# Optimization experiments

Measured on AMD Instinct MI355X. Metric: run time of the kernel, lower is better.

Reference implementation:

```python
import jax, jax.numpy as jnp
import numpy as np

N = 8192      # total nodes
B = 8         # graphs in batch
L = 1024      # nodes per graph (max_len)
E = 262144    # edges (before self loops)
IN = 64       # in_channels
H = 8         # heads
C = 32        # hidden_channels (per-head out dim)
D = H * C     # 256, d_model
DFF = 2048    # transformer FFN dim (torch default)
NEG = -1e9


def setup_inputs() -> dict:
    key = jax.random.key(0)
    ks = jax.random.split(key, 24)
    def p(i, shape):
        return jax.random.normal(ks[i], shape, jnp.float32) * 0.02
    x = jax.random.normal(ks[0], (N, IN), jnp.float32)
    src = jax.random.randint(ks[1], (E,), 0, N)
    dst = (src // L) * L + jax.random.randint(ks[2], (E,), 0, L)  # keep edges within a graph
    edge_index = jnp.stack([src, dst]).astype(jnp.int32)
    batch = (jnp.arange(N) // L).astype(jnp.int32)
    return dict(
        x=x, edge_index=edge_index, batch=batch,
        gat_W0=p(3, (D, IN)), gat_W12=p(4, (2, D, D)),
        gat_att_src=p(5, (3, H, C)), gat_att_dst=p(6, (3, H, C)), gat_bias=p(7, (3, D)),
        tf_qkv_w=p(8, (2, 3 * D, D)), tf_qkv_b=p(9, (2, 3 * D)),
        tf_out_w=p(10, (2, D, D)), tf_out_b=p(11, (2, D)),
        tf_ln1_w=jnp.ones((2, D)), tf_ln1_b=jnp.zeros((2, D)),
        tf_ln2_w=jnp.ones((2, D)), tf_ln2_b=jnp.zeros((2, D)),
        tf_ff1_w=p(12, (2, DFF, D)), tf_ff1_b=p(13, (2, DFF)),
        tf_ff2_w=p(14, (2, D, DFF)), tf_ff2_b=p(15, (2, D)),
        pred_w=p(16, (3, D)), pred_b=p(17, (3,)),
    )


def _gat(x, src, dst, W, att_s, att_d, bias):
    # PyG GATConv, concat=True, add_self_loops (appended in caller), eval (no dropout)
    h = (x @ W.T).reshape(-1, H, C)                       # [N,H,C]
    a_s = (h * att_s).sum(-1)                             # [N,H]
    a_d = (h * att_d).sum(-1)
    e = jax.nn.leaky_relu(a_s[src] + a_d[dst], 0.2)       # [E+N,H]
    m = jax.ops.segment_max(e, dst, num_segments=N)       # per-dst softmax
    e = jnp.exp(e - m[dst])
    s = jax.ops.segment_sum(e, dst, num_segments=N)
    alpha = e / s[dst]
    out = jax.ops.segment_sum(h[src] * alpha[..., None], dst, num_segments=N)
    return out.reshape(-1, D) + bias


def _ln(x, w, b):
    mu = x.mean(-1, keepdims=True)
    v = ((x - mu) ** 2).mean(-1, keepdims=True)
    return (x - mu) / jnp.sqrt(v + 1e-5) * w + b


def _tf_layer(x, mask, qkv_w, qkv_b, out_w, out_b, ln1w, ln1b, ln2w, ln2b, f1w, f1b, f2w, f2b):
    # torch TransformerEncoderLayer (post-LN, relu), key padding mask, eval mode
    qkv = x @ qkv_w.T + qkv_b                              # [B,L,3D]
    q, k, v = jnp.split(qkv, 3, -1)
    sh = lambda t: t.reshape(B, L, H, D // H)
    q, k, v = sh(q), sh(k), sh(v)
    sc = jnp.einsum('bqhd,bkhd->bhqk', q, k) * (1.0 / float(np.sqrt(D // H)))
    sc = jnp.where(mask[:, None, None, :], NEG, sc)
    a = jax.nn.softmax(sc, -1)
    o = jnp.einsum('bhqk,bkhd->bqhd', a, v).reshape(B, L, D)
    x = _ln(x + o @ out_w.T + out_b, ln1w, ln1b)
    f = jax.nn.relu(x @ f1w.T + f1b) @ f2w.T + f2b
    return _ln(x + f, ln2w, ln2b)


def reference(x, edge_index, batch, gat_W0, gat_W12, gat_att_src, gat_att_dst, gat_bias,
              tf_qkv_w, tf_qkv_b, tf_out_w, tf_out_b, tf_ln1_w, tf_ln1_b, tf_ln2_w, tf_ln2_b,
              tf_ff1_w, tf_ff1_b, tf_ff2_w, tf_ff2_b, pred_w, pred_b):
    loops = jnp.arange(N, dtype=edge_index.dtype)
    src = jnp.concatenate([edge_index[0], loops])
    dst = jnp.concatenate([edge_index[1], loops])
    h = jax.nn.relu(_gat(x, src, dst, gat_W0, gat_att_src[0], gat_att_dst[0], gat_bias[0]))
    for i in range(2):
        h = jax.nn.relu(_gat(h, src, dst, gat_W12[i], gat_att_src[i + 1], gat_att_dst[i + 1], gat_bias[i + 1]))
    # ragged -> padded [B, L, D] (vectorized scatter instead of python loop)
    seq_lens = jax.ops.segment_sum(jnp.ones(N, jnp.int32), batch, num_segments=B)
    starts = jnp.cumsum(seq_lens) - seq_lens
    pos = jnp.arange(N) - starts[batch]
    xp = jnp.zeros((B, L, D), h.dtype).at[batch, pos].set(h)
    mask = jnp.arange(L)[None, :] >= seq_lens[:, None]     # True = padded key
    for i in range(2):
        xp = _tf_layer(xp, mask, tf_qkv_w[i], tf_qkv_b[i], tf_out_w[i], tf_out_b[i],
                       tf_ln1_w[i], tf_ln1_b[i], tf_ln2_w[i], tf_ln2_b[i],
                       tf_ff1_w[i], tf_ff1_b[i], tf_ff2_w[i], tf_ff2_b[i])
    return xp @ pred_w.T + pred_b                          # [B,L,3]
```

## Files before the change

kernel.cpp:

```cpp
#include <hip/hip_runtime.h>
#include <hip/hip_bf16.h>

#define NN 8192
#define EE 262144
#define BB 8
#define LL 1024
#define HH 8
#define DD 256
#define DFFN 2048

typedef short s8v __attribute__((ext_vector_type(8)));
typedef float f32x4 __attribute__((ext_vector_type(4)));
typedef unsigned short ushort;

__device__ inline ushort f2bf(float f) {
    unsigned u = __float_as_uint(f);
    u = (u + 0x7fffu + ((u >> 16) & 1u)) >> 16;
    return (ushort)u;
}
__device__ inline float bf2f(ushort u) {
    return __uint_as_float(((unsigned)u) << 16);
}

template<bool BIAS, bool RELU, bool RES, bool WF, bool WB>
__global__ __launch_bounds__(256) void mgemm_kernel(
    const ushort* __restrict__ A, const ushort* __restrict__ W,
    const float* __restrict__ bias, const float* __restrict__ res,
    float* __restrict__ Cf, ushort* __restrict__ Cb, int M, int N, int K)
{
    __shared__ ushort As[128 * 32];
    __shared__ ushort Bs[128 * 32];
    int t = threadIdx.x;
    int l = t & 63;
    int quad = l >> 4, l15 = l & 15;
    int swz = (l15 >> 1) & 3;
    int rq = (quad ^ swz) * 8;
    int w = t >> 6;
    int wm = (w >> 1) * 64, wn = (w & 1) * 64;
    int m0 = blockIdx.x * 128, n0 = blockIdx.y * 128;

    f32x4 z = {0.f, 0.f, 0.f, 0.f};
    f32x4 acc[4][4];
#pragma unroll
    for (int i = 0; i < 4; ++i)
#pragma unroll
        for (int j = 0; j < 4; ++j) acc[i][j] = z;

    for (int k0 = 0; k0 < K; k0 += 32) {
#pragma unroll
        for (int i = 0; i < 2; ++i) {
            int chunk = i * 256 + t;
            int r = chunk >> 2, q = chunk & 3;
            int qs = (q ^ ((r >> 1) & 3)) * 8;
            __builtin_amdgcn_global_load_lds(
                (const __attribute__((address_space(1))) unsigned int*)
                    (A + (size_t)(m0 + r) * K + k0 + qs),
                (__attribute__((address_space(3))) unsigned int*)(As + chunk * 8), 16, 0, 0);
            __builtin_amdgcn_global_load_lds(
                (const __attribute__((address_space(1))) unsigned int*)
                    (W + (size_t)(n0 + r) * K + k0 + qs),
                (__attribute__((address_space(3))) unsigned int*)(Bs + chunk * 8), 16, 0, 0);
        }
        __syncthreads();
        s8v af[4], bfv[4];
#pragma unroll
        for (int i = 0; i < 4; ++i) {
            af[i]  = *(const s8v*)(As + (wm + i * 16 + l15) * 32 + rq);
            bfv[i] = *(const s8v*)(Bs + (wn + i * 16 + l15) * 32 + rq);
        }
#pragma unroll
        for (int mi = 0; mi < 4; ++mi)
#pragma unroll
            for (int ni = 0; ni < 4; ++ni)
                acc[mi][ni] = __builtin_amdgcn_mfma_f32_16x16x32_bf16(
                    af[mi], bfv[ni], acc[mi][ni], 0, 0, 0);
        __syncthreads();
    }

#pragma unroll
    for (int mi = 0; mi < 4; ++mi) {
#pragma unroll
        for (int ni = 0; ni < 4; ++ni) {
            int n = n0 + wn + ni * 16 + l15;
#pragma unroll
            for (int r = 0; r < 4; ++r) {
                int m = m0 + wm + mi * 16 + quad * 4 + r;
                float v = acc[mi][ni][r];
                if (BIAS) v += bias[n];
                if (RES)  v += res[(size_t)m * N + n];
                if (RELU) v = fmaxf(v, 0.f);
                if (WF) Cf[(size_t)m * N + n] = v;
                if (WB) Cb[(size_t)m * N + n] = f2bf(v);
            }
        }
    }
}

template<bool BIAS, bool RELU, bool RES, bool WF, bool WB, bool ASD>
__global__ __launch_bounds__(256) void mgemm64_kernel(
    const ushort* __restrict__ A, const ushort* __restrict__ W,
    const float* __restrict__ bias, const float* __restrict__ res,
    float* __restrict__ Cf, ushort* __restrict__ Cb,
    const float* __restrict__ atts, const float* __restrict__ attd,
    float* __restrict__ a_s, float* __restrict__ a_d, int M, int N, int K)
{
    __shared__ ushort As[64 * 32];
    __shared__ ushort Bs[64 * 32];
    int t = threadIdx.x;
    int l = t & 63;
    int quad = l >> 4, l15 = l & 15;
    int rq = (quad ^ ((l15 >> 1) & 3)) * 8;
    int w = t >> 6;
    int wm = (w >> 1) * 32, wn = (w & 1) * 32;
    int m0 = blockIdx.x * 64, n0 = blockIdx.y * 64;

    f32x4 z = {0.f, 0.f, 0.f, 0.f};
    f32x4 acc[2][2];
#pragma unroll
    for (int i = 0; i < 2; ++i)
#pragma unroll
        for (int j = 0; j < 2; ++j) acc[i][j] = z;

    for (int k0 = 0; k0 < K; k0 += 32) {
        {
            int r = t >> 2, q = t & 3;
            int qs = (q ^ ((r >> 1) & 3)) * 8;
            __builtin_amdgcn_global_load_lds(
                (const __attribute__((address_space(1))) unsigned int*)
                    (A + (size_t)(m0 + r) * K + k0 + qs),
                (__attribute__((address_space(3))) unsigned int*)(As + t * 8), 16, 0, 0);
            __builtin_amdgcn_global_load_lds(
                (const __attribute__((address_space(1))) unsigned int*)
                    (W + (size_t)(n0 + r) * K + k0 + qs),
                (__attribute__((address_space(3))) unsigned int*)(Bs + t * 8), 16, 0, 0);
        }
        __syncthreads();
        s8v af[2], bfv[2];
#pragma unroll
        for (int i = 0; i < 2; ++i) {
            af[i]  = *(const s8v*)(As + (wm + i * 16 + l15) * 32 + rq);
            bfv[i] = *(const s8v*)(Bs + (wn + i * 16 + l15) * 32 + rq);
        }
#pragma unroll
        for (int mi = 0; mi < 2; ++mi)
#pragma unroll
            for (int ni = 0; ni < 2; ++ni)
                acc[mi][ni] = __builtin_amdgcn_mfma_f32_16x16x32_bf16(
                    af[mi], bfv[ni], acc[mi][ni], 0, 0, 0);
        __syncthreads();
    }

#pragma unroll
    for (int mi = 0; mi < 2; ++mi) {
#pragma unroll
        for (int ni = 0; ni < 2; ++ni) {
            int n = n0 + wn + ni * 16 + l15;
#pragma unroll
            for (int r = 0; r < 4; ++r) {
                int m = m0 + wm + mi * 16 + quad * 4 + r;
                float v = acc[mi][ni][r];
                if (BIAS) v += bias[n];
                if (RES)  v += res[(size_t)m * N + n];
                if (RELU) v = fmaxf(v, 0.f);
                if (WF) Cf[(size_t)m * N + n] = v;
                if (WB) Cb[(size_t)m * N + n] = f2bf(v);
            }
        }
    }

    if (ASD) {
        int head = ((n0 + wn) >> 5) & 7;
        float as0 = atts[head * 32 + l15];
        float as1 = atts[head * 32 + 16 + l15];
        float ad0 = attd[head * 32 + l15];
        float ad1 = attd[head * 32 + 16 + l15];
#pragma unroll
        for (int mi = 0; mi < 2; ++mi)
#pragma unroll
            for (int r = 0; r < 4; ++r) {
                float sp = acc[mi][0][r] * as0 + acc[mi][1][r] * as1;
                float dp = acc[mi][0][r] * ad0 + acc[mi][1][r] * ad1;
#pragma unroll
                for (int off = 1; off < 16; off <<= 1) {
                    sp += __shfl_xor(sp, off);
                    dp += __shfl_xor(dp, off);
                }
                if (l15 == 0) {
                    int m = m0 + wm + mi * 16 + quad * 4 + r;
                    a_s[m * 8 + head] = sp;
                    a_d[m * 8 + head] = dp;
                }
            }
    }
}

__global__ __launch_bounds__(256) void mgemm_qkv_kernel(
    const ushort* __restrict__ A, const ushort* __restrict__ W,
    const float* __restrict__ bias,
    ushort* __restrict__ Qb, ushort* __restrict__ Kb, ushort* __restrict__ Vt,
    int M, int K)
{
    __shared__ ushort As[128 * 32];
    __shared__ ushort Bs[128 * 32];
    int t = threadIdx.x;
    int l = t & 63;
    int quad = l >> 4, l15 = l & 15;
    int swz = (l15 >> 1) & 3;
    int rq = (quad ^ swz) * 8;
    int w = t >> 6;
    int wm = (w >> 1) * 64, wn = (w & 1) * 64;
    int m0 = blockIdx.x * 128, n0 = blockIdx.y * 128;

    f32x4 z = {0.f, 0.f, 0.f, 0.f};
    f32x4 acc[4][4];
#pragma unroll
    for (int i = 0; i < 4; ++i)
#pragma unroll
        for (int j = 0; j < 4; ++j) acc[i][j] = z;

    for (int k0 = 0; k0 < K; k0 += 32) {
#pragma unroll
        for (int i = 0; i < 2; ++i) {
            int chunk = i * 256 + t;
            int r = chunk >> 2, q = chunk & 3;
            int qs = (q ^ ((r >> 1) & 3)) * 8;
            __builtin_amdgcn_global_load_lds(
                (const __attribute__((address_space(1))) unsigned int*)
                    (A + (size_t)(m0 + r) * K + k0 + qs),
                (__attribute__((address_space(3))) unsigned int*)(As + chunk * 8), 16, 0, 0);
            __builtin_amdgcn_global_load_lds(
                (const __attribute__((address_space(1))) unsigned int*)
                    (W + (size_t)(n0 + r) * K + k0 + qs),
                (__attribute__((address_space(3))) unsigned int*)(Bs + chunk * 8), 16, 0, 0);
        }
        __syncthreads();
        s8v af[4], bfv[4];
#pragma unroll
        for (int i = 0; i < 4; ++i) {
            af[i]  = *(const s8v*)(As + (wm + i * 16 + l15) * 32 + rq);
            bfv[i] = *(const s8v*)(Bs + (wn + i * 16 + l15) * 32 + rq);
        }
#pragma unroll
        for (int mi = 0; mi < 4; ++mi)
#pragma unroll
            for (int ni = 0; ni < 4; ++ni)
                acc[mi][ni] = __builtin_amdgcn_mfma_f32_16x16x32_bf16(
                    af[mi], bfv[ni], acc[mi][ni], 0, 0, 0);
        __syncthreads();
    }

#pragma unroll
    for (int mi = 0; mi < 4; ++mi) {
#pragma unroll
        for (int ni = 0; ni < 4; ++ni) {
            int n = n0 + wn + ni * 16 + l15;
            int sec = n >> 8, hc = n & 255;
            int hh = hc >> 5, c = hc & 31;
            float bv = bias[n];
#pragma unroll
            for (int r = 0; r < 4; ++r) {
                int m = m0 + wm + mi * 16 + quad * 4 + r;
                float v = acc[mi][ni][r] + bv;
                int b = m >> 10, ll2 = m & 1023;
                int bh = b * 8 + hh;
                if (sec == 0)
                    Qb[(size_t)bh * 32768 + ll2 * 32 + c] = f2bf(v * 0.17677669529663687f);
                else if (sec == 1)
                    Kb[(size_t)bh * 32768 + ll2 * 32 + c] = f2bf(v);
                else
                    Vt[(size_t)bh * 32768 + c * 1024 + ll2] = f2bf(v);
            }
        }
    }
}

__global__ __launch_bounds__(256) void castall_kernel(
    const float* __restrict__ W0, const float* __restrict__ W12,
    const float* __restrict__ qkvw, const float* __restrict__ outw,
    const float* __restrict__ f1w, const float* __restrict__ f2w,
    const float* __restrict__ x,
    ushort* __restrict__ W0b, ushort* __restrict__ W12b,
    ushort* __restrict__ qkvb, ushort* __restrict__ outb,
    ushort* __restrict__ f1b, ushort* __restrict__ f2b,
    ushort* __restrict__ xb, int* __restrict__ deg)
{
    int tid = blockIdx.x * 256 + threadIdx.x;
    if (tid < 2048) *(int4*)(deg + tid * 4) = make_int4(0, 0, 0, 0);
    int e = tid * 4;
    if (e >= 3293184) return;
    const float* s; ushort* d; int off;
    if (e < 16384)        { s = W0;   d = W0b;  off = e; }
    else if (e < 147456)  { s = W12;  d = W12b; off = e - 16384; }
    else if (e < 540672)  { s = qkvw; d = qkvb; off = e - 147456; }
    else if (e < 671744)  { s = outw; d = outb; off = e - 540672; }
    else if (e < 1720320) { s = f1w;  d = f1b;  off = e - 671744; }
    else if (e < 2768896) { s = f2w;  d = f2b;  off = e - 1720320; }
    else                  { s = x;    d = xb;   off = e - 2768896; }
    float4 v = *(const float4*)(s + off);
    d[off + 0] = f2bf(v.x); d[off + 1] = f2bf(v.y);
    d[off + 2] = f2bf(v.z); d[off + 3] = f2bf(v.w);
}

__global__ void count_kernel(const int* __restrict__ ei, int* __restrict__ deg)
{
    int e = blockIdx.x * 256 + threadIdx.x;
    if (e >= EE + NN) return;
    int d = (e < EE) ? ei[EE + e] : (e - EE);
    atomicAdd(&deg[d], 1);
}

__global__ __launch_bounds__(1024) void scan_kernel(
    const int* __restrict__ deg, int* __restrict__ rowptr, int* __restrict__ cursor)
{
    __shared__ int part[1024];
    int t = threadIdx.x;
    int base = t * 8;
    int loc[8]; int s = 0;
#pragma unroll
    for (int i = 0; i < 8; ++i) { loc[i] = deg[base + i]; s += loc[i]; }
    part[t] = s;
    __syncthreads();
    for (int off = 1; off < 1024; off <<= 1) {
        int v = (t >= off) ? part[t - off] : 0;
        __syncthreads();
        part[t] += v;
        __syncthreads();
    }
    int run = (t == 0) ? 0 : part[t - 1];
#pragma unroll
    for (int i = 0; i < 8; ++i) { rowptr[base + i] = run; cursor[base + i] = run; run += loc[i]; }
    if (t == 1023) rowptr[NN] = run;
}

__global__ void scatter_kernel(const int* __restrict__ ei, int* __restrict__ cursor,
                               int* __restrict__ col)
{
    int e = blockIdx.x * 256 + threadIdx.x;
    if (e >= EE + NN) return;
    int s, d;
    if (e < EE) { s = ei[e]; d = ei[EE + e]; } else { s = e - EE; d = s; }
    int slot = atomicAdd(&cursor[d], 1);
    col[slot] = s;
}

__global__ __launch_bounds__(256) void gat_agg_kernel(
    const ushort* __restrict__ hlinb, const float* __restrict__ a_s,
    const float* __restrict__ a_d, const int* __restrict__ rowptr,
    const int* __restrict__ col, const float* __restrict__ bias,
    float* __restrict__ alpha_e,
    float* __restrict__ out, ushort* __restrict__ outb)
{
    int wid = threadIdx.x >> 6, lane = threadIdx.x & 63;
    int dst = blockIdx.x * 4 + wid;
    int start = rowptr[dst], end = rowptr[dst + 1];
    float ad[HH];
#pragma unroll
    for (int h = 0; h < HH; ++h) ad[h] = a_d[(size_t)dst * HH + h];

    float sm[HH];
#pragma unroll
    for (int h = 0; h < HH; ++h) sm[h] = 0.f;
    for (int e = start + lane; e < end; e += 64) {
        int s = col[e];
        float* al = alpha_e + (size_t)e * HH;
#pragma unroll
        for (int h = 0; h < HH; ++h) {
            float v = a_s[(size_t)s * HH + h] + ad[h];
            v = v > 0.f ? v : 0.2f * v;
            float p = __expf(v);
            sm[h] += p;
            al[h] = p;
        }
    }
#pragma unroll
    for (int h = 0; h < HH; ++h)
#pragma unroll
        for (int off = 32; off; off >>= 1) sm[h] += __shfl_xor(sm[h], off);

    int myh = lane >> 3;
    float invs = 1.f / sm[myh];
    float a0 = 0.f, a1 = 0.f, a2 = 0.f, a3 = 0.f;
    for (int e = start; e < end; ++e) {
        int s = col[e];
        float alpha = alpha_e[(size_t)e * HH + myh] * invs;
        uint2 hv = *(const uint2*)(hlinb + (size_t)s * DD + lane * 4);
        a0 += alpha * bf2f((ushort)(hv.x & 0xffff));
        a1 += alpha * bf2f((ushort)(hv.x >> 16));
        a2 += alpha * bf2f((ushort)(hv.y & 0xffff));
        a3 += alpha * bf2f((ushort)(hv.y >> 16));
    }
    float4 bv = *(const float4*)(bias + lane * 4);
    float r0 = fmaxf(a0 + bv.x, 0.f);
    float r1 = fmaxf(a1 + bv.y, 0.f);
    float r2 = fmaxf(a2 + bv.z, 0.f);
    float r3 = fmaxf(a3 + bv.w, 0.f);
    float* op = out + (size_t)dst * DD + lane * 4;
    op[0] = r0; op[1] = r1; op[2] = r2; op[3] = r3;
    ushort* ob = outb + (size_t)dst * DD + lane * 4;
    ob[0] = f2bf(r0); ob[1] = f2bf(r1); ob[2] = f2bf(r2); ob[3] = f2bf(r3);
}

__global__ __launch_bounds__(256, 4) void attn_flash_kernel(
    const ushort* __restrict__ Qb, const ushort* __restrict__ Kb,
    const ushort* __restrict__ Vt, ushort* __restrict__ outb)
{
    __shared__ ushort Ks[128 * 32];
    __shared__ ushort Vs[32 * 128];
    __shared__ ushort pw[4][16][132];

    int t = threadIdx.x;
    int w = t >> 6, lane = t & 63;
    int quad = lane >> 4, l15 = lane & 15;
    int kq = (quad ^ ((l15 >> 1) & 3)) * 8;
    int bh = blockIdx.y;
    int q0 = blockIdx.x * 64 + w * 16;
    int b = bh >> 3, h = bh & 7;

    const ushort* qbase = Qb + (size_t)bh * 32768;
    const ushort* kbase = Kb + (size_t)bh * 32768;
    const ushort* vbase = Vt + (size_t)bh * 32768;

    s8v aq = *(const s8v*)(qbase + (q0 + l15) * 32 + quad * 8);

    f32x4 z = {0.f, 0.f, 0.f, 0.f};
    f32x4 o0 = z, o1 = z;
    float lden[4] = {0.f, 0.f, 0.f, 0.f};

    for (int ch = 0; ch < 8; ++ch) {
        int j0 = ch * 128;
#pragma unroll
        for (int i = 0; i < 2; ++i) {
            int idx = i * 256 + t;
            int kr = idx >> 2, kc = idx & 3;
            int kcs = (kc ^ ((kr >> 1) & 3)) * 8;
            __builtin_amdgcn_global_load_lds(
                (const __attribute__((address_space(1))) unsigned int*)
                    (kbase + (size_t)(j0 + kr) * 32 + kcs),
                (__attribute__((address_space(3))) unsigned int*)(Ks + idx * 8), 16, 0, 0);
            int vr = idx >> 4, vc = idx & 15;
            int vcs = (vc ^ (vr & 15)) * 8;
            __builtin_amdgcn_global_load_lds(
                (const __attribute__((address_space(1))) unsigned int*)
                    (vbase + (size_t)vr * 1024 + j0 + vcs),
                (__attribute__((address_space(3))) unsigned int*)(Vs + idx * 8), 16, 0, 0);
        }
        __syncthreads();

        f32x4 s[8];
#pragma unroll
        for (int kk = 0; kk < 8; ++kk) {
            s8v bk = *(const s8v*)(Ks + (kk * 16 + l15) * 32 + kq);
            s[kk] = __builtin_amdgcn_mfma_f32_16x16x32_bf16(aq, bk, z, 0, 0, 0);
        }

        float cs[4] = {0.f, 0.f, 0.f, 0.f};
#pragma unroll
        for (int kk = 0; kk < 8; ++kk) {
#pragma unroll
            for (int r = 0; r < 4; ++r) {
                float p = __expf(s[kk][r]);
                cs[r] += p;
                pw[w][quad * 4 + r][kk * 16 + l15] = f2bf(p);
            }
        }
#pragma unroll
        for (int r = 0; r < 4; ++r) {
#pragma unroll
            for (int off = 1; off < 16; off <<= 1) cs[r] += __shfl_xor(cs[r], off);
            lden[r] += cs[r];
        }

#pragma unroll
        for (int kk = 0; kk < 4; ++kk) {
            s8v ap = *(const s8v*)(&pw[w][l15][kk * 32 + quad * 8]);
            int c0 = ((kk * 4 + quad) ^ l15) * 8;
            s8v b0 = *(const s8v*)(Vs + (size_t)l15 * 128 + c0);
            s8v b1 = *(const s8v*)(Vs + (size_t)(16 + l15) * 128 + c0);
            o0 = __builtin_amdgcn_mfma_f32_16x16x32_bf16(ap, b0, o0, 0, 0, 0);
            o1 = __builtin_amdgcn_mfma_f32_16x16x32_bf16(ap, b1, o1, 0, 0, 0);
        }
        __syncthreads();
    }

#pragma unroll
    for (int r = 0; r < 4; ++r) {
        int row = q0 + quad * 4 + r;
        float inv = 1.f / lden[r];
        outb[(size_t)(b * 1024 + row) * 256 + h * 32 + l15]      = f2bf(o0[r] * inv);
        outb[(size_t)(b * 1024 + row) * 256 + h * 32 + 16 + l15] = f2bf(o1[r] * inv);
    }
}

__global__ __launch_bounds__(256) void ln_kernel(
    float* __restrict__ x, const float* __restrict__ w, const float* __restrict__ b,
    ushort* __restrict__ xb)
{
    int wid = threadIdx.x >> 6, lane = threadIdx.x & 63;
    size_t row = blockIdx.x * 4 + wid;
    float4 v = *(float4*)(x + row * DD + lane * 4);
    float s = v.x + v.y + v.z + v.w;
#pragma unroll
    for (int off = 32; off; off >>= 1) s += __shfl_xor(s, off);
    float mu = s * (1.f / 256.f);
    float dx = v.x - mu, dy = v.y - mu, dz = v.z - mu, dw = v.w - mu;
    float q = dx * dx + dy * dy + dz * dz + dw * dw;
#pragma unroll
    for (int off = 32; off; off >>= 1) q += __shfl_xor(q, off);
    float rstd = rsqrtf(q * (1.f / 256.f) + 1e-5f);
    int c = lane * 4;
    float4 wv = *(const float4*)(w + c);
    float4 bv = *(const float4*)(b + c);
    float4 o;
    o.x = dx * rstd * wv.x + bv.x;
    o.y = dy * rstd * wv.y + bv.y;
    o.z = dz * rstd * wv.z + bv.z;
    o.w = dw * rstd * wv.w + bv.w;
    *(float4*)(x + row * DD + c) = o;
    ushort* ob = xb + row * DD + c;
    ob[0] = f2bf(o.x); ob[1] = f2bf(o.y); ob[2] = f2bf(o.z); ob[3] = f2bf(o.w);
}

__global__ __launch_bounds__(256) void ln_pred_kernel(
    const float* __restrict__ x, const float* __restrict__ w, const float* __restrict__ b,
    const float* __restrict__ pw, const float* __restrict__ pb,
    float* __restrict__ out)
{
    int wid = threadIdx.x >> 6, lane = threadIdx.x & 63;
    size_t row = blockIdx.x * 4 + wid;
    float4 v = *(const float4*)(x + row * DD + lane * 4);
    float s = v.x + v.y + v.z + v.w;
#pragma unroll
    for (int off = 32; off; off >>= 1) s += __shfl_xor(s, off);
    float mu = s * (1.f / 256.f);
    float dx = v.x - mu, dy = v.y - mu, dz = v.z - mu, dw = v.w - mu;
    float q = dx * dx + dy * dy + dz * dz + dw * dw;
#pragma unroll
    for (int off = 32; off; off >>= 1) q += __shfl_xor(q, off);
    float rstd = rsqrtf(q * (1.f / 256.f) + 1e-5f);
    int c = lane * 4;
    float4 wv = *(const float4*)(w + c);
    float4 bv = *(const float4*)(b + c);
    float4 o;
    o.x = dx * rstd * wv.x + bv.x;
    o.y = dy * rstd * wv.y + bv.y;
    o.z = dz * rstd * wv.z + bv.z;
    o.w = dw * rstd * wv.w + bv.w;
    float4 w0 = *(const float4*)(pw + c);
    float4 w1 = *(const float4*)(pw + DD + c);
    float4 w2 = *(const float4*)(pw + 2 * DD + c);
    float s0 = o.x * w0.x + o.y * w0.y + o.z * w0.z + o.w * w0.w;
    float s1 = o.x * w1.x + o.y * w1.y + o.z * w1.z + o.w * w1.w;
    float s2 = o.x * w2.x + o.y * w2.y + o.z * w2.z + o.w * w2.w;
#pragma unroll
    for (int off = 32; off; off >>= 1) {
        s0 += __shfl_xor(s0, off);
        s1 += __shfl_xor(s1, off);
        s2 += __shfl_xor(s2, off);
    }
    if (lane == 0) {
        out[row * 3 + 0] = s0 + pb[0];
        out[row * 3 + 1] = s1 + pb[1];
        out[row * 3 + 2] = s2 + pb[2];
    }
}

extern "C" void kernel_launch(void* const* d_in, const int* in_sizes, int n_in,
                              void* d_out, int out_size, void* d_ws, size_t ws_size,
                              hipStream_t stream)
{
    const float* x        = (const float*)d_in[0];
    const int*   ei       = (const int*)d_in[1];
    const float* gat_W0   = (const float*)d_in[3];
    const float* gat_W12  = (const float*)d_in[4];
    const float* att_src  = (const float*)d_in[5];
    const float* att_dst  = (const float*)d_in[6];
    const float* gat_bias = (const float*)d_in[7];
    const float* qkv_w    = (const float*)d_in[8];
    const float* qkv_b    = (const float*)d_in[9];
    const float* out_w    = (const float*)d_in[10];
    const float* out_b    = (const float*)d_in[11];
    const float* ln1_w    = (const float*)d_in[12];
    const float* ln1_b    = (const float*)d_in[13];
    const float* ln2_w    = (const float*)d_in[14];
    const float* ln2_b    = (const float*)d_in[15];
    const float* ff1_w    = (const float*)d_in[16];
    const float* ff1_b    = (const float*)d_in[17];
    const float* ff2_w    = (const float*)d_in[18];
    const float* ff2_b    = (const float*)d_in[19];
    const float* pred_w   = (const float*)d_in[20];
    const float* pred_b   = (const float*)d_in[21];
    float* outp = (float*)d_out;

    float* ws   = (float*)d_ws;
    float* hA   = ws;
    float* hB   = ws + 2097152;
    ushort* ffb  = (ushort*)(ws + 4194304);
    ushort* Qb   = (ushort*)(ws + 12582912);
    ushort* Kb   = (ushort*)(ws + 13631488);
    ushort* Vt   = (ushort*)(ws + 14680064);
    ushort* attnb= (ushort*)(ws + 15728640);
    ushort* lnb  = (ushort*)(ws + 16777216);
    ushort* hBb  = (ushort*)(ws + 17825792);
    ushort* xb   = (ushort*)(ws + 18874368);
    ushort* wbase= (ushort*)(ws + 19136512);
    ushort* W0b    = wbase;
    ushort* W12b   = wbase + 16384;
    ushort* qkv_wb = wbase + 147456;
    ushort* out_wb = wbase + 540672;
    ushort* ff1_wb = wbase + 671744;
    ushort* ff2_wb = wbase + 1720320;
    float* a_s  = ws + 20520960;
    float* a_d  = ws + 20586496;
    int*   iw   = (int*)(ws + 20652032);
    int*   deg    = iw;
    int*   rowptr = iw + 8192;
    int*   cursor = iw + 16392;
    int*   col    = iw + 24592;
    ushort* hAb    = (ushort*)(ws + 21000192);
    float*  alpha_e = ws + 22048768;

    castall_kernel<<<3216, 256, 0, stream>>>(
        gat_W0, gat_W12, qkv_w, out_w, ff1_w, ff2_w, x,
        W0b, W12b, qkv_wb, out_wb, ff1_wb, ff2_wb, xb, deg);

    int etot = EE + NN;
    count_kernel<<<(etot + 255) / 256, 256, 0, stream>>>(ei, deg);
    scan_kernel<<<1, 1024, 0, stream>>>(deg, rowptr, cursor);
    scatter_kernel<<<(etot + 255) / 256, 256, 0, stream>>>(ei, cursor, col);

    mgemm64_kernel<false, false, false, false, true, true><<<dim3(128, 4), 256, 0, stream>>>(
        xb, W0b, nullptr, nullptr, nullptr, hAb, att_src, att_dst, a_s, a_d, NN, DD, 64);
    gat_agg_kernel<<<2048, 256, 0, stream>>>(hAb, a_s, a_d, rowptr, col, gat_bias,
                                             alpha_e, hB, hBb);

    for (int l = 0; l < 2; ++l) {
        mgemm64_kernel<false, false, false, false, true, true><<<dim3(128, 4), 256, 0, stream>>>(
            hBb, W12b + (size_t)l * DD * DD, nullptr, nullptr, nullptr, hAb,
            att_src + (l + 1) * 256, att_dst + (l + 1) * 256, a_s, a_d, NN, DD, DD);
        gat_agg_kernel<<<2048, 256, 0, stream>>>(
            hAb, a_s, a_d, rowptr, col, gat_bias + (l + 1) * 256, alpha_e, hB, hBb);
    }

    for (int l = 0; l < 2; ++l) {
        mgemm_qkv_kernel<<<dim3(64, 6), 256, 0, stream>>>(
            hBb, qkv_wb + (size_t)l * 768 * DD, qkv_b + l * 768, Qb, Kb, Vt, NN, DD);
        attn_flash_kernel<<<dim3(16, 64), 256, 0, stream>>>(Qb, Kb, Vt, attnb);
        mgemm64_kernel<true, false, true, true, false, false><<<dim3(128, 4), 256, 0, stream>>>(
            attnb, out_wb + (size_t)l * DD * DD, out_b + l * DD, hB,
            hA, nullptr, nullptr, nullptr, nullptr, nullptr, NN, DD, DD);
        ln_kernel<<<2048, 256, 0, stream>>>(hA, ln1_w + l * DD, ln1_b + l * DD, lnb);
        mgemm_kernel<true, true, false, false, true><<<dim3(64, 16), 256, 0, stream>>>(
            lnb, ff1_wb + (size_t)l * DFFN * DD, ff1_b + l * DFFN, nullptr,
            nullptr, ffb, NN, DFFN, DD);
        mgemm64_kernel<true, false, true, true, false, false><<<dim3(128, 4), 256, 0, stream>>>(
            ffb, ff2_wb + (size_t)l * DD * DFFN, ff2_b + l * DD, hA,
            hB, nullptr, nullptr, nullptr, nullptr, nullptr, NN, DD, DFFN);
        if (l == 0) {
            ln_kernel<<<2048, 256, 0, stream>>>(hB, ln2_w + l * DD, ln2_b + l * DD, hBb);
        } else {
            ln_pred_kernel<<<2048, 256, 0, stream>>>(
                hB, ln2_w + l * DD, ln2_b + l * DD, pred_w, pred_b, outp);
        }
    }
}
```

Measured before the change: 471.6 us.

## Retile GEMMs to K=64 steps and process 32 query rows per attention wave

Result: faster. 451.7 us (-4.2%).

```diff
diff --git a/kernel.cpp b/kernel.cpp
--- a/kernel.cpp
+++ b/kernel.cpp
@@ -104,12 +104,12 @@
     const float* __restrict__ atts, const float* __restrict__ attd,
     float* __restrict__ a_s, float* __restrict__ a_d, int M, int N, int K)
 {
-    __shared__ ushort As[64 * 32];
-    __shared__ ushort Bs[64 * 32];
+    __shared__ ushort As[64 * 64];
+    __shared__ ushort Bs[64 * 64];
     int t = threadIdx.x;
     int l = t & 63;
     int quad = l >> 4, l15 = l & 15;
-    int rq = (quad ^ ((l15 >> 1) & 3)) * 8;
+    int r7 = l15 & 7;
     int w = t >> 6;
     int wm = (w >> 1) * 32, wn = (w & 1) * 32;
     int m0 = blockIdx.x * 64, n0 = blockIdx.y * 64;
@@ -121,32 +121,39 @@
 #pragma unroll
         for (int j = 0; j < 2; ++j) acc[i][j] = z;
 
-    for (int k0 = 0; k0 < K; k0 += 32) {
-        {
-            int r = t >> 2, q = t & 3;
-            int qs = (q ^ ((r >> 1) & 3)) * 8;
+    for (int k0 = 0; k0 < K; k0 += 64) {
+#pragma unroll
+        for (int i = 0; i < 2; ++i) {
+            int chunk = i * 256 + t;
+            int r = chunk >> 3, p = chunk & 7;
+            int qs = (p ^ (r & 7)) * 8;
             __builtin_amdgcn_global_load_lds(
                 (const __attribute__((address_space(1))) unsigned int*)
                     (A + (size_t)(m0 + r) * K + k0 + qs),
-                (__attribute__((address_space(3))) unsigned int*)(As + t * 8), 16, 0, 0);
+                (__attribute__((address_space(3))) unsigned int*)(As + chunk * 8), 16, 0, 0);
             __builtin_amdgcn_global_load_lds(
                 (const __attribute__((address_space(1))) unsigned int*)
                     (W + (size_t)(n0 + r) * K + k0 + qs),
-                (__attribute__((address_space(3))) unsigned int*)(Bs + t * 8), 16, 0, 0);
-        }
-        __syncthreads();
-        s8v af[2], bfv[2];
-#pragma unroll
-        for (int i = 0; i < 2; ++i) {
-            af[i]  = *(const s8v*)(As + (wm + i * 16 + l15) * 32 + rq);
-            bfv[i] = *(const s8v*)(Bs + (wn + i * 16 + l15) * 32 + rq);
-        }
-#pragma unroll
-        for (int mi = 0; mi < 2; ++mi)
-#pragma unroll
-            for (int ni = 0; ni < 2; ++ni)
-                acc[mi][ni] = __builtin_amdgcn_mfma_f32_16x16x32_bf16(
-                    af[mi], bfv[ni], acc[mi][ni], 0, 0, 0);
+                (__attribute__((address_space(3))) unsigned int*)(Bs + chunk * 8), 16, 0, 0);
+        }
+        __syncthreads();
+#pragma unroll
+        for (int kk = 0; kk < 2; ++kk) {
+            s8v af[2], bfv[2];
+            int c = kk * 4 + quad;
+            int off = (c ^ r7) * 8;
+#pragma unroll
+            for (int i = 0; i < 2; ++i) {
+                af[i]  = *(const s8v*)(As + (wm + i * 16 + l15) * 64 + off);
+                bfv[i] = *(const s8v*)(Bs + (wn + i * 16 + l15) * 64 + off);
+            }
+#pragma unroll
+            for (int mi = 0; mi < 2; ++mi)
+#pragma unroll
+                for (int ni = 0; ni < 2; ++ni)
+                    acc[mi][ni] = __builtin_amdgcn_mfma_f32_16x16x32_bf16(
+                        af[mi], bfv[ni], acc[mi][ni], 0, 0, 0);
+        }
         __syncthreads();
     }
 
@@ -200,30 +207,29 @@
     ushort* __restrict__ Qb, ushort* __restrict__ Kb, ushort* __restrict__ Vt,
     int M, int K)
 {
-    __shared__ ushort As[128 * 32];
-    __shared__ ushort Bs[128 * 32];
+    __shared__ ushort As[64 * 64];
+    __shared__ ushort Bs[64 * 64];
     int t = threadIdx.x;
     int l = t & 63;
     int quad = l >> 4, l15 = l & 15;
-    int swz = (l15 >> 1) & 3;
-    int rq = (quad ^ swz) * 8;
+    int r7 = l15 & 7;
     int w = t >> 6;
-    int wm = (w >> 1) * 64, wn = (w & 1) * 64;
-    int m0 = blockIdx.x * 128, n0 = blockIdx.y * 128;
+    int wm = (w >> 1) * 32, wn = (w & 1) * 32;
+    int m0 = blockIdx.x * 64, n0 = blockIdx.y * 64;
 
     f32x4 z = {0.f, 0.f, 0.f, 0.f};
-    f32x4 acc[4][4];
-#pragma unroll
-    for (int i = 0; i < 4; ++i)
-#pragma unroll
-        for (int j = 0; j < 4; ++j) acc[i][j] = z;
-
-    for (int k0 = 0; k0 < K; k0 += 32) {
+    f32x4 acc[2][2];
+#pragma unroll
+    for (int i = 0; i < 2; ++i)
+#pragma unroll
+        for (int j = 0; j < 2; ++j) acc[i][j] = z;
+
+    for (int k0 = 0; k0 < K; k0 += 64) {
 #pragma unroll
         for (int i = 0; i < 2; ++i) {
             int chunk = i * 256 + t;
-            int r = chunk >> 2, q = chunk & 3;
-            int qs = (q ^ ((r >> 1) & 3)) * 8;
+            int r = chunk >> 3, p = chunk & 7;
+            int qs = (p ^ (r & 7)) * 8;
             __builtin_amdgcn_global_load_lds(
                 (const __attribute__((address_space(1))) unsigned int*)
                     (A + (size_t)(m0 + r) * K + k0 + qs),
@@ -234,25 +240,30 @@
                 (__attribute__((address_space(3))) unsigned int*)(Bs + chunk * 8), 16, 0, 0);
         }
         __syncthreads();
-        s8v af[4], bfv[4];
-#pragma unroll
-        for (int i = 0; i < 4; ++i) {
-            af[i]  = *(const s8v*)(As + (wm + i * 16 + l15) * 32 + rq);
-            bfv[i] = *(const s8v*)(Bs + (wn + i * 16 + l15) * 32 + rq);
-        }
-#pragma unroll
-        for (int mi = 0; mi < 4; ++mi)
-#pragma unroll
-            for (int ni = 0; ni < 4; ++ni)
-                acc[mi][ni] = __builtin_amdgcn_mfma_f32_16x16x32_bf16(
-                    af[mi], bfv[ni], acc[mi][ni], 0, 0, 0);
-        __syncthreads();
-    }
-
-#pragma unroll
-    for (int mi = 0; mi < 4; ++mi) {
-#pragma unroll
-        for (int ni = 0; ni < 4; ++ni) {
+#pragma unroll
+        for (int kk = 0; kk < 2; ++kk) {
+            s8v af[2], bfv[2];
+            int c = kk * 4 + quad;
+            int off = (c ^ r7) * 8;
+#pragma unroll
+            for (int i = 0; i < 2; ++i) {
+                af[i]  = *(const s8v*)(As + (wm + i * 16 + l15) * 64 + off);
+                bfv[i] = *(const s8v*)(Bs + (wn + i * 16 + l15) * 64 + off);
+            }
+#pragma unroll
+            for (int mi = 0; mi < 2; ++mi)
+#pragma unroll
+                for (int ni = 0; ni < 2; ++ni)
+                    acc[mi][ni] = __builtin_amdgcn_mfma_f32_16x16x32_bf16(
+                        af[mi], bfv[ni], acc[mi][ni], 0, 0, 0);
+        }
+        __syncthreads();
+    }
+
+#pragma unroll
+    for (int mi = 0; mi < 2; ++mi) {
+#pragma unroll
+        for (int ni = 0; ni < 2; ++ni) {
             int n = n0 + wn + ni * 16 + l15;
             int sec = n >> 8, hc = n & 255;
             int hh = hc >> 5, c = hc & 31;
@@ -400,31 +411,33 @@
     ob[0] = f2bf(r0); ob[1] = f2bf(r1); ob[2] = f2bf(r2); ob[3] = f2bf(r3);
 }
 
-__global__ __launch_bounds__(256, 4) void attn_flash_kernel(
+__global__ __launch_bounds__(256, 2) void attn_flash_kernel(
     const ushort* __restrict__ Qb, const ushort* __restrict__ Kb,
     const ushort* __restrict__ Vt, ushort* __restrict__ outb)
 {
     __shared__ ushort Ks[128 * 32];
     __shared__ ushort Vs[32 * 128];
-    __shared__ ushort pw[4][16][132];
+    __shared__ ushort pw[4][32][132];
 
     int t = threadIdx.x;
     int w = t >> 6, lane = t & 63;
     int quad = lane >> 4, l15 = lane & 15;
     int kq = (quad ^ ((l15 >> 1) & 3)) * 8;
     int bh = blockIdx.y;
-    int q0 = blockIdx.x * 64 + w * 16;
+    int q0 = blockIdx.x * 128 + w * 32;
     int b = bh >> 3, h = bh & 7;
 
     const ushort* qbase = Qb + (size_t)bh * 32768;
     const ushort* kbase = Kb + (size_t)bh * 32768;
     const ushort* vbase = Vt + (size_t)bh * 32768;
 
-    s8v aq = *(const s8v*)(qbase + (q0 + l15) * 32 + quad * 8);
+    s8v aq0 = *(const s8v*)(qbase + (q0 + l15) * 32 + quad * 8);
+    s8v aq1 = *(const s8v*)(qbase + (q0 + 16 + l15) * 32 + quad * 8);
 
     f32x4 z = {0.f, 0.f, 0.f, 0.f};
-    f32x4 o0 = z, o1 = z;
-    float lden[4] = {0.f, 0.f, 0.f, 0.f};
+    f32x4 o00 = z, o01 = z, o10 = z, o11 = z;
+    float lden0[4] = {0.f, 0.f, 0.f, 0.f};
+    float lden1[4] = {0.f, 0.f, 0.f, 0.f};
 
     for (int ch = 0; ch < 8; ++ch) {
         int j0 = ch * 128;
@@ -446,48 +459,64 @@
         }
         __syncthreads();
 
-        f32x4 s[8];
+        f32x4 s0[8], s1[8];
 #pragma unroll
         for (int kk = 0; kk < 8; ++kk) {
             s8v bk = *(const s8v*)(Ks + (kk * 16 + l15) * 32 + kq);
-            s[kk] = __builtin_amdgcn_mfma_f32_16x16x32_bf16(aq, bk, z, 0, 0, 0);
-        }
-
-        float cs[4] = {0.f, 0.f, 0.f, 0.f};
+            s0[kk] = __builtin_amdgcn_mfma_f32_16x16x32_bf16(aq0, bk, z, 0, 0, 0);
+            s1[kk] = __builtin_amdgcn_mfma_f32_16x16x32_bf16(aq1, bk, z, 0, 0, 0);
+        }
+
+        float cs0[4] = {0.f, 0.f, 0.f, 0.f};
+        float cs1[4] = {0.f, 0.f, 0.f, 0.f};
 #pragma unroll
         for (int kk = 0; kk < 8; ++kk) {
 #pragma unroll
             for (int r = 0; r < 4; ++r) {
-                float p = __expf(s[kk][r]);
-                cs[r] += p;
-                pw[w][quad * 4 + r][kk * 16 + l15] = f2bf(p);
+                float p0 = __expf(s0[kk][r]);
+                float p1 = __expf(s1[kk][r]);
+                cs0[r] += p0;
+                cs1[r] += p1;
+                pw[w][quad * 4 + r][kk * 16 + l15]      = f2bf(p0);
+                pw[w][16 + quad * 4 + r][kk * 16 + l15] = f2bf(p1);
             }
         }
 #pragma unroll
         for (int r = 0; r < 4; ++r) {
 #pragma unroll
-            for (int off = 1; off < 16; off <<= 1) cs[r] += __shfl_xor(cs[r], off);
-            lden[r] += cs[r];
+            for (int off = 1; off < 16; off <<= 1) {
+                cs0[r] += __shfl_xor(cs0[r], off);
+                cs1[r] += __shfl_xor(cs1[r], off);
+            }
+            lden0[r] += cs0[r];
+            lden1[r] += cs1[r];
         }
 
 #pragma unroll
         for (int kk = 0; kk < 4; ++kk) {
-            s8v ap = *(const s8v*)(&pw[w][l15][kk * 32 + quad * 8]);
+            s8v ap0 = *(const s8v*)(&pw[w][l15][kk * 32 + quad * 8]);
+            s8v ap1 = *(const s8v*)(&pw[w][16 + l15][kk * 32 + quad * 8]);
             int c0 = ((kk * 4 + quad) ^ l15) * 8;
             s8v b0 = *(const s8v*)(Vs + (size_t)l15 * 128 + c0);
             s8v b1 = *(const s8v*)(Vs + (size_t)(16 + l15) * 128 + c0);
-            o0 = __builtin_amdgcn_mfma_f32_16x16x32_bf16(ap, b0, o0, 0, 0, 0);
-            o1 = __builtin_amdgcn_mfma_f32_16x16x32_bf16(ap, b1, o1, 0, 0, 0);
+            o00 = __builtin_amdgcn_mfma_f32_16x16x32_bf16(ap0, b0, o00, 0, 0, 0);
+            o01 = __builtin_amdgcn_mfma_f32_16x16x32_bf16(ap0, b1, o01, 0, 0, 0);
+            o10 = __builtin_amdgcn_mfma_f32_16x16x32_bf16(ap1, b0, o10, 0, 0, 0);
+            o11 = __builtin_amdgcn_mfma_f32_16x16x32_bf16(ap1, b1, o11, 0, 0, 0);
         }
         __syncthreads();
     }
 
 #pragma unroll
     for (int r = 0; r < 4; ++r) {
-        int row = q0 + quad * 4 + r;
-        float inv = 1.f / lden[r];
-        outb[(size_t)(b * 1024 + row) * 256 + h * 32 + l15]      = f2bf(o0[r] * inv);
-        outb[(size_t)(b * 1024 + row) * 256 + h * 32 + 16 + l15] = f2bf(o1[r] * inv);
+        int row0 = q0 + quad * 4 + r;
+        int row1 = row0 + 16;
+        float i0 = 1.f / lden0[r];
+        float i1 = 1.f / lden1[r];
+        outb[(size_t)(b * 1024 + row0) * 256 + h * 32 + l15]      = f2bf(o00[r] * i0);
+        outb[(size_t)(b * 1024 + row0) * 256 + h * 32 + 16 + l15] = f2bf(o01[r] * i0);
+        outb[(size_t)(b * 1024 + row1) * 256 + h * 32 + l15]      = f2bf(o10[r] * i1);
+        outb[(size_t)(b * 1024 + row1) * 256 + h * 32 + 16 + l15] = f2bf(o11[r] * i1);
     }
 }
 
@@ -642,9 +671,9 @@
     }
 
     for (int l = 0; l < 2; ++l) {
-        mgemm_qkv_kernel<<<dim3(64, 6), 256, 0, stream>>>(
+        mgemm_qkv_kernel<<<dim3(128, 12), 256, 0, stream>>>(
             hBb, qkv_wb + (size_t)l * 768 * DD, qkv_b + l * 768, Qb, Kb, Vt, NN, DD);
-        attn_flash_kernel<<<dim3(16, 64), 256, 0, stream>>>(Qb, Kb, Vt, attnb);
+        attn_flash_kernel<<<dim3(8, 64), 256, 0, stream>>>(Qb, Kb, Vt, attnb);
         mgemm64_kernel<true, false, true, true, false, false><<<dim3(128, 4), 256, 0, stream>>>(
             attnb, out_wb + (size_t)l * DD * DD, out_b + l * DD, hB,
             hA, nullptr, nullptr, nullptr, nullptr, nullptr, NN, DD, DD);
```
